# Kernel tuning notes

Measured on AMD Instinct MI355X. Metric: run time of the kernel, lower is better.

## Reference

```python
import jax, jax.numpy as jnp
import numpy as np

KSZ = 3      # kernel_size
NH = 4       # num_heads


def setup_inputs() -> dict:
    key = jax.random.key(0)
    ks = jax.random.split(key, 4)
    B, D, H, W, C = 1, 28, 28, 28, 192
    N = D * H * W
    s = 0.02  # trunc_normal std used by the module's init
    return {
        "x": jax.random.normal(ks[0], (B, N, C), jnp.float32),
        "Wq": jax.random.normal(ks[1], (C, C), jnp.float32) * s,
        "bq": jnp.zeros((C,), jnp.float32),
        "Wkv": jax.random.normal(ks[2], (C, 2 * C), jnp.float32) * s,
        "bkv": jnp.zeros((2 * C,), jnp.float32),
        "Wp": jax.random.normal(ks[3], (C, C), jnp.float32) * s,
        "bp": jnp.zeros((C,), jnp.float32),
        "D": D, "H": H, "W": W,
    }


def _windows(t, D, H, W):
    # t: (B, D+2, H+2, W+2, nh, hc) zero-padded; gather the 27 neighborhood
    # offsets (same flattening order as unfold: d-major, then h, then w).
    return jnp.stack(
        [t[:, dz:dz + D, dy:dy + H, dx:dx + W]
         for dz in range(KSZ) for dy in range(KSZ) for dx in range(KSZ)],
        axis=4)  # (B, D, H, W, 27, nh, hc)


def reference(x, Wq, bq, Wkv, bkv, Wp, bp, D, H, W):
    B, N, C = x.shape
    hc = C // NH
    scale = hc ** (-0.5)
    xv = x.reshape(B, D, H, W, C)

    q = (xv @ Wq + bq).reshape(B, D, H, W, NH, hc) * scale
    kv = (xv @ Wkv + bkv).reshape(B, D, H, W, 2, NH, hc)
    k, v = kv[..., 0, :, :], kv[..., 1, :, :]

    pad = ((0, 0), (1, 1), (1, 1), (1, 1), (0, 0), (0, 0))
    kwin = _windows(jnp.pad(k, pad), D, H, W)  # (B,D,H,W,27,nh,hc)
    vwin = _windows(jnp.pad(v, pad), D, H, W)

    # per-voxel 1x27 attention over the 3x3x3 neighborhood
    attn = jnp.einsum('bdhwnc,bdhwknc->bdhwnk', q, kwin)
    attn = jax.nn.softmax(attn, axis=-1)
    out = jnp.einsum('bdhwnk,bdhwknc->bdhwnc', attn, vwin)
    out = out.reshape(B, D, H, W, C) @ Wp + bp
    return out.reshape(B, N, C)
```

## Files before the change

kernel.cpp:

```cpp
#include <hip/hip_runtime.h>
#include <math.h>

#define CDIM 192
#define DD 28
#define NVOX (DD * DD * DD)

typedef __attribute__((ext_vector_type(8))) short bf16x8;
typedef __attribute__((ext_vector_type(4))) float f32x4;

__device__ __forceinline__ float bf2f(unsigned short u) {
  union { unsigned int i; float f; } w; w.i = ((unsigned int)u) << 16; return w.f;
}
__device__ __forceinline__ float blo(unsigned int u) {
  union { unsigned int i; float f; } w; w.i = u << 16; return w.f;
}
__device__ __forceinline__ float bhi(unsigned int u) {
  union { unsigned int i; float f; } w; w.i = u & 0xffff0000u; return w.f;
}
__device__ __forceinline__ unsigned short f2bf(float f) {
  union { float ff; unsigned int i; } w; w.ff = f;
  unsigned int x = w.i;
  return (unsigned short)((x + 0x7fffu + ((x >> 16) & 1u)) >> 16);
}

__global__ __launch_bounds__(256) void prep(
    const float* __restrict__ x, const float* __restrict__ Wq,
    const float* __restrict__ Wkv, const float* __restrict__ Wp,
    unsigned short* __restrict__ xb, unsigned short* __restrict__ WqT,
    unsigned short* __restrict__ WkvT, unsigned short* __restrict__ WpT)
{
  const int XU = NVOX * CDIM / 8;
  const int t = blockIdx.x * 256 + threadIdx.x;
  if (t < XU) {
    const float4 a = ((const float4*)x)[t * 2];
    const float4 b = ((const float4*)x)[t * 2 + 1];
    unsigned short o[8] = {f2bf(a.x), f2bf(a.y), f2bf(a.z), f2bf(a.w),
                           f2bf(b.x), f2bf(b.y), f2bf(b.z), f2bf(b.w)};
    *(uint4*)(&xb[t * 8]) = *(const uint4*)o;
  } else {
    int u = t - XU;
    if (u < CDIM * CDIM) {
      const int n = u / CDIM, k = u % CDIM;
      WqT[u] = f2bf(Wq[k * CDIM + n]);
    } else if ((u -= CDIM * CDIM) < 2 * CDIM * CDIM) {
      const int n = u / CDIM, k = u % CDIM;
      WkvT[u] = f2bf(Wkv[k * 2 * CDIM + n]);
    } else {
      u -= 2 * CDIM * CDIM;
      const int n = u / CDIM, k = u % CDIM;
      WpT[u] = f2bf(Wp[k * CDIM + n]);
    }
  }
}

template<int OUT_BF16>
__global__ __launch_bounds__(256) void gemm_bf16(
    const unsigned short* __restrict__ A,
    const unsigned short* __restrict__ Bt,
    const float* __restrict__ bias,
    void* __restrict__ Cout,
    int N, float alpha)
{
  __shared__ unsigned short As[64 * 200];
  __shared__ unsigned short Bs[64 * 200];
  const int tid = threadIdx.x;
  const int n0 = blockIdx.x * 64;
  const int m0 = blockIdx.y * 64;

#pragma unroll
  for (int u = tid; u < 1536; u += 256) {
    const int row = u / 24, c = (u % 24) * 8;
    *(uint4*)(&As[row * 200 + c]) =
        *(const uint4*)(&A[(size_t)(m0 + row) * CDIM + c]);
    *(uint4*)(&Bs[row * 200 + c]) =
        *(const uint4*)(&Bt[(size_t)(n0 + row) * CDIM + c]);
  }
  __syncthreads();

  const int l = tid & 63, w = tid >> 6;
  const int wm = (w >> 1) * 32, wn = (w & 1) * 32;
  const int lr = l & 15, lk = (l >> 4) * 8;

  f32x4 acc[2][2] = {};
  const unsigned short* pa = &As[(wm + lr) * 200 + lk];
  const unsigned short* pb = &Bs[(wn + lr) * 200 + lk];

#pragma unroll
  for (int k0 = 0; k0 < CDIM; k0 += 32) {
    const bf16x8 a0 = *(const bf16x8*)(pa + k0);
    const bf16x8 a1 = *(const bf16x8*)(pa + 16 * 200 + k0);
    const bf16x8 b0 = *(const bf16x8*)(pb + k0);
    const bf16x8 b1 = *(const bf16x8*)(pb + 16 * 200 + k0);
    acc[0][0] = __builtin_amdgcn_mfma_f32_16x16x32_bf16(a0, b0, acc[0][0], 0, 0, 0);
    acc[0][1] = __builtin_amdgcn_mfma_f32_16x16x32_bf16(a0, b1, acc[0][1], 0, 0, 0);
    acc[1][0] = __builtin_amdgcn_mfma_f32_16x16x32_bf16(a1, b0, acc[1][0], 0, 0, 0);
    acc[1][1] = __builtin_amdgcn_mfma_f32_16x16x32_bf16(a1, b1, acc[1][1], 0, 0, 0);
  }

#pragma unroll
  for (int i = 0; i < 2; ++i)
#pragma unroll
    for (int j = 0; j < 2; ++j) {
      const int gc = n0 + wn + j * 16 + lr;
      const float bv = bias[gc];
#pragma unroll
      for (int r = 0; r < 4; ++r) {
        const int gr = m0 + wm + i * 16 + (l >> 4) * 4 + r;
        const float v = (acc[i][j][r] + bv) * alpha;
        if (OUT_BF16)
          ((unsigned short*)Cout)[(size_t)gr * N + gc] = f2bf(v);
        else
          ((float*)Cout)[(size_t)gr * N + gc] = v;
      }
    }
}

__global__ __launch_bounds__(256, 4) void attn3d_line(
    const unsigned short* __restrict__ q,
    const unsigned short* __restrict__ kv,
    unsigned short* __restrict__ y)
{
  const int bid = blockIdx.x;
  const int zy = (bid & 7) * 98 + (bid >> 3);
  const int z = zy / 28, yr = zy % 28;
  const int h = threadIdx.x >> 6;
  const int lane = threadIdx.x & 63;
  const int x = lane & 31;
  const int g = lane >> 5;
  const int xc = x < 28 ? x : 27;
  const int cb = h * 48 + g * 24;
  const int vox = (z * 28 + yr) * 28 + xc;

  float qf[24];
  {
    const uint4* qp = (const uint4*)(q + (size_t)vox * CDIM + cb);
    const uint4 a = qp[0], b = qp[1], c = qp[2];
    const unsigned int uu[12] = {a.x, a.y, a.z, a.w, b.x, b.y, b.z, b.w,
                                 c.x, c.y, c.z, c.w};
#pragma unroll
    for (int i = 0; i < 12; ++i) { qf[2*i] = blo(uu[i]); qf[2*i+1] = bhi(uu[i]); }
  }

  const int nx = 3 - (x == 0) - (x == 27);
  const int nyv = 3 - (yr == 0) - (yr == 27);
  const int nzv = 3 - (z == 0) - (z == 27);
  const int noob = 27 - nx * nyv * nzv;
  float m = noob ? 0.f : -INFINITY;
  float s = (float)noob;
  float out[24];
#pragma unroll
  for (int i = 0; i < 24; ++i) out[i] = 0.f;

  const int lm1 = lane - 1, lp1 = lane + 1;
  const bool okm = (x > 0), okp = (x < 27);

  for (int dz = -1; dz <= 1; ++dz) {
    const int zz = z + dz;
    if ((unsigned)zz >= 28u) continue;
    for (int dy = -1; dy <= 1; ++dy) {
      const int yv = yr + dy;
      if ((unsigned)yv >= 28u) continue;
      const unsigned short* row =
          kv + (size_t)((zz * 28 + yv) * 28 + xc) * (2 * CDIM) + cb;
      const uint4* kp = (const uint4*)row;
      const uint4* vp = (const uint4*)(row + CDIM);
      const uint4 ka = kp[0], kb = kp[1], kc = kp[2];
      const uint4 va = vp[0], vb = vp[1], vc = vp[2];
      const unsigned int ku[12] = {ka.x, ka.y, ka.z, ka.w, kb.x, kb.y, kb.z,
                                   kb.w, kc.x, kc.y, kc.z, kc.w};
      const unsigned int vu[12] = {va.x, va.y, va.z, va.w, vb.x, vb.y, vb.z,
                                   vb.w, vc.x, vc.y, vc.z, vc.w};

      float p0 = 0.f, p1 = 0.f, p2 = 0.f;
#pragma unroll
      for (int i = 0; i < 12; ++i) {
        p1 += qf[2*i] * blo(ku[i]) + qf[2*i+1] * bhi(ku[i]);
        unsigned int t = (unsigned int)__shfl((int)ku[i], lm1);
        p0 += qf[2*i] * blo(t) + qf[2*i+1] * bhi(t);
        t = (unsigned int)__shfl((int)ku[i], lp1);
        p2 += qf[2*i] * blo(t) + qf[2*i+1] * bhi(t);
      }
      p0 += __shfl_xor(p0, 32);
      p1 += __shfl_xor(p1, 32);
      p2 += __shfl_xor(p2, 32);

      const float l0 = okm ? p0 : -INFINITY;
      const float l2 = okp ? p2 : -INFINITY;
      const float nm = fmaxf(m, fmaxf(p1, fmaxf(l0, l2)));
      const float sc = __expf(m - nm);
      const float w0 = okm ? __expf(p0 - nm) : 0.f;
      const float w1 = __expf(p1 - nm);
      const float w2 = okp ? __expf(p2 - nm) : 0.f;
      s = s * sc + w0 + w1 + w2;
      m = nm;

#pragma unroll
      for (int i = 0; i < 12; ++i) {
        const unsigned int am = (unsigned int)__shfl((int)vu[i], lm1);
        const unsigned int ap = (unsigned int)__shfl((int)vu[i], lp1);
        out[2*i]   = out[2*i]   * sc + w0 * blo(am) + w1 * blo(vu[i]) + w2 * blo(ap);
        out[2*i+1] = out[2*i+1] * sc + w0 * bhi(am) + w1 * bhi(vu[i]) + w2 * bhi(ap);
      }
    }
  }

  if (x < 28) {
    const float inv = 1.f / s;
    unsigned int ou[12];
#pragma unroll
    for (int i = 0; i < 12; ++i)
      ou[i] = (unsigned int)f2bf(out[2*i] * inv) |
              ((unsigned int)f2bf(out[2*i+1] * inv) << 16);
    uint4* yp = (uint4*)(y + (size_t)vox * CDIM + cb);
    yp[0] = make_uint4(ou[0], ou[1], ou[2], ou[3]);
    yp[1] = make_uint4(ou[4], ou[5], ou[6], ou[7]);
    yp[2] = make_uint4(ou[8], ou[9], ou[10], ou[11]);
  }
}

extern "C" void kernel_launch(void* const* d_in, const int* in_sizes, int n_in,
                              void* d_out, int out_size, void* d_ws, size_t ws_size,
                              hipStream_t stream) {
  const float* x   = (const float*)d_in[0];
  const float* Wq  = (const float*)d_in[1];
  const float* bq  = (const float*)d_in[2];
  const float* Wkv = (const float*)d_in[3];
  const float* bkv = (const float*)d_in[4];
  const float* Wp  = (const float*)d_in[5];
  const float* bp  = (const float*)d_in[6];
  float* out = (float*)d_out;

  unsigned short* xb   = (unsigned short*)d_ws;
  unsigned short* WqT  = xb + (size_t)NVOX * CDIM;
  unsigned short* WkvT = WqT + CDIM * CDIM;
  unsigned short* WpT  = WkvT + 2 * CDIM * CDIM;
  unsigned short* qb   = WpT + CDIM * CDIM;
  unsigned short* kvb  = qb + (size_t)NVOX * CDIM;
  unsigned short* yb   = kvb + (size_t)NVOX * 2 * CDIM;

  const float scale = 1.0f / sqrtf(48.0f);

  prep<<<674304 / 256, 256, 0, stream>>>(x, Wq, Wkv, Wp, xb, WqT, WkvT, WpT);

  gemm_bf16<1><<<dim3(CDIM / 64, NVOX / 64), 256, 0, stream>>>(
      xb, WqT, bq, qb, CDIM, scale);
  gemm_bf16<1><<<dim3(2 * CDIM / 64, NVOX / 64), 256, 0, stream>>>(
      xb, WkvT, bkv, kvb, 2 * CDIM, 1.0f);
  attn3d_line<<<DD * DD, 256, 0, stream>>>(qb, kvb, yb);
  gemm_bf16<0><<<dim3(CDIM / 64, NVOX / 64), 256, 0, stream>>>(
      yb, WpT, bp, out, CDIM, 1.0f);
}
```

Baseline: 147.5 us.

## Fuse x conversion into merged QKV GEMM and software-pipeline attention row loads

Removes the separate pass that converts x to bf16 and instead converts fp32 x into shared memory inside a merged QKV GEMM. That GEMM reuses each A tile across several N tiles, with the attention scale folded into the prepared weights and biases. The attention kernel now double-buffers K/V row loads across the nine neighbor rows, loading the next row before computing the current one, and drops the occupancy hint from launch bounds. This cuts global traffic and launches, but the QKV GEMM has fewer blocks with serialized N tiles, and the attention kernel uses more registers.

```diff
diff --git a/kernel.cpp b/kernel.cpp
--- a/kernel.cpp
+++ b/kernel.cpp
@@ -8,9 +8,6 @@
 typedef __attribute__((ext_vector_type(8))) short bf16x8;
 typedef __attribute__((ext_vector_type(4))) float f32x4;
 
-__device__ __forceinline__ float bf2f(unsigned short u) {
-  union { unsigned int i; float f; } w; w.i = ((unsigned int)u) << 16; return w.f;
-}
 __device__ __forceinline__ float blo(unsigned int u) {
   union { unsigned int i; float f; } w; w.i = u << 16; return w.f;
 }
@@ -23,99 +20,151 @@
   return (unsigned short)((x + 0x7fffu + ((x >> 16) & 1u)) >> 16);
 }
 
-__global__ __launch_bounds__(256) void prep(
-    const float* __restrict__ x, const float* __restrict__ Wq,
-    const float* __restrict__ Wkv, const float* __restrict__ Wp,
-    unsigned short* __restrict__ xb, unsigned short* __restrict__ WqT,
-    unsigned short* __restrict__ WkvT, unsigned short* __restrict__ WpT)
+__global__ __launch_bounds__(256) void prep_w(
+    const float* __restrict__ Wq, const float* __restrict__ Wkv,
+    const float* __restrict__ Wp, const float* __restrict__ bq,
+    const float* __restrict__ bkv,
+    unsigned short* __restrict__ WqkvT, unsigned short* __restrict__ WpT,
+    float* __restrict__ biasAll, float scale)
 {
-  const int XU = NVOX * CDIM / 8;
-  const int t = blockIdx.x * 256 + threadIdx.x;
-  if (t < XU) {
-    const float4 a = ((const float4*)x)[t * 2];
-    const float4 b = ((const float4*)x)[t * 2 + 1];
-    unsigned short o[8] = {f2bf(a.x), f2bf(a.y), f2bf(a.z), f2bf(a.w),
-                           f2bf(b.x), f2bf(b.y), f2bf(b.z), f2bf(b.w)};
-    *(uint4*)(&xb[t * 8]) = *(const uint4*)o;
-  } else {
-    int u = t - XU;
-    if (u < CDIM * CDIM) {
-      const int n = u / CDIM, k = u % CDIM;
-      WqT[u] = f2bf(Wq[k * CDIM + n]);
-    } else if ((u -= CDIM * CDIM) < 2 * CDIM * CDIM) {
-      const int n = u / CDIM, k = u % CDIM;
-      WkvT[u] = f2bf(Wkv[k * 2 * CDIM + n]);
-    } else {
-      u -= 2 * CDIM * CDIM;
-      const int n = u / CDIM, k = u % CDIM;
-      WpT[u] = f2bf(Wp[k * CDIM + n]);
-    }
-  }
-}
-
-template<int OUT_BF16>
-__global__ __launch_bounds__(256) void gemm_bf16(
-    const unsigned short* __restrict__ A,
+  int t = blockIdx.x * 256 + threadIdx.x;
+  if (t < 576 * CDIM) {
+    const int n = t / CDIM, k = t % CDIM;
+    const float v = (n < CDIM) ? Wq[k * CDIM + n] * scale
+                               : Wkv[k * 2 * CDIM + (n - CDIM)];
+    WqkvT[t] = f2bf(v);
+    return;
+  }
+  t -= 576 * CDIM;
+  if (t < CDIM * CDIM) {
+    const int n = t / CDIM, k = t % CDIM;
+    WpT[t] = f2bf(Wp[k * CDIM + n]);
+    return;
+  }
+  t -= CDIM * CDIM;
+  if (t < 576)
+    biasAll[t] = (t < CDIM) ? bq[t] * scale : bkv[t - CDIM];
+}
+
+__global__ __launch_bounds__(256) void gemm_qkv(
+    const float* __restrict__ X,
     const unsigned short* __restrict__ Bt,
-    const float* __restrict__ bias,
-    void* __restrict__ Cout,
-    int N, float alpha)
+    const float* __restrict__ biasAll,
+    unsigned short* __restrict__ qb,
+    unsigned short* __restrict__ kvb)
 {
   __shared__ unsigned short As[64 * 200];
   __shared__ unsigned short Bs[64 * 200];
   const int tid = threadIdx.x;
-  const int n0 = blockIdx.x * 64;
-  const int m0 = blockIdx.y * 64;
+  const int m0 = blockIdx.x * 64;
+  const int by = blockIdx.y;
 
 #pragma unroll
   for (int u = tid; u < 1536; u += 256) {
     const int row = u / 24, c = (u % 24) * 8;
-    *(uint4*)(&As[row * 200 + c]) =
-        *(const uint4*)(&A[(size_t)(m0 + row) * CDIM + c]);
-    *(uint4*)(&Bs[row * 200 + c]) =
-        *(const uint4*)(&Bt[(size_t)(n0 + row) * CDIM + c]);
-  }
-  __syncthreads();
+    const float4 f0 = *(const float4*)(&X[(size_t)(m0 + row) * CDIM + c]);
+    const float4 f1 = *(const float4*)(&X[(size_t)(m0 + row) * CDIM + c + 4]);
+    unsigned short o[8] = {f2bf(f0.x), f2bf(f0.y), f2bf(f0.z), f2bf(f0.w),
+                           f2bf(f1.x), f2bf(f1.y), f2bf(f1.z), f2bf(f1.w)};
+    *(uint4*)(&As[row * 200 + c]) = *(const uint4*)o;
+  }
 
   const int l = tid & 63, w = tid >> 6;
   const int wm = (w >> 1) * 32, wn = (w & 1) * 32;
   const int lr = l & 15, lk = (l >> 4) * 8;
-
-  f32x4 acc[2][2] = {};
   const unsigned short* pa = &As[(wm + lr) * 200 + lk];
   const unsigned short* pb = &Bs[(wn + lr) * 200 + lk];
 
-#pragma unroll
-  for (int k0 = 0; k0 < CDIM; k0 += 32) {
-    const bf16x8 a0 = *(const bf16x8*)(pa + k0);
-    const bf16x8 a1 = *(const bf16x8*)(pa + 16 * 200 + k0);
-    const bf16x8 b0 = *(const bf16x8*)(pb + k0);
-    const bf16x8 b1 = *(const bf16x8*)(pb + 16 * 200 + k0);
-    acc[0][0] = __builtin_amdgcn_mfma_f32_16x16x32_bf16(a0, b0, acc[0][0], 0, 0, 0);
-    acc[0][1] = __builtin_amdgcn_mfma_f32_16x16x32_bf16(a0, b1, acc[0][1], 0, 0, 0);
-    acc[1][0] = __builtin_amdgcn_mfma_f32_16x16x32_bf16(a1, b0, acc[1][0], 0, 0, 0);
-    acc[1][1] = __builtin_amdgcn_mfma_f32_16x16x32_bf16(a1, b1, acc[1][1], 0, 0, 0);
-  }
-
-#pragma unroll
-  for (int i = 0; i < 2; ++i)
-#pragma unroll
-    for (int j = 0; j < 2; ++j) {
-      const int gc = n0 + wn + j * 16 + lr;
-      const float bv = bias[gc];
-#pragma unroll
-      for (int r = 0; r < 4; ++r) {
-        const int gr = m0 + wm + i * 16 + (l >> 4) * 4 + r;
-        const float v = (acc[i][j][r] + bv) * alpha;
-        if (OUT_BF16)
-          ((unsigned short*)Cout)[(size_t)gr * N + gc] = f2bf(v);
-        else
-          ((float*)Cout)[(size_t)gr * N + gc] = v;
+  for (int nt = by; nt < 9; nt += 2) {
+    const int n0 = nt * 64;
+    __syncthreads();
+#pragma unroll
+    for (int u = tid; u < 1536; u += 256) {
+      const int row = u / 24, c = (u % 24) * 8;
+      *(uint4*)(&Bs[row * 200 + c]) =
+          *(const uint4*)(&Bt[(size_t)(n0 + row) * CDIM + c]);
+    }
+    __syncthreads();
+
+    f32x4 acc[2][2] = {};
+#pragma unroll
+    for (int k0 = 0; k0 < CDIM; k0 += 32) {
+      const bf16x8 a0 = *(const bf16x8*)(pa + k0);
+      const bf16x8 a1 = *(const bf16x8*)(pa + 16 * 200 + k0);
+      const bf16x8 b0 = *(const bf16x8*)(pb + k0);
+      const bf16x8 b1 = *(const bf16x8*)(pb + 16 * 200 + k0);
+      acc[0][0] = __builtin_amdgcn_mfma_f32_16x16x32_bf16(a0, b0, acc[0][0], 0, 0, 0);
+      acc[0][1] = __builtin_amdgcn_mfma_f32_16x16x32_bf16(a0, b1, acc[0][1], 0, 0, 0);
+      acc[1][0] = __builtin_amdgcn_mfma_f32_16x16x32_bf16(a1, b0, acc[1][0], 0, 0, 0);
+      acc[1][1] = __builtin_amdgcn_mfma_f32_16x16x32_bf16(a1, b1, acc[1][1], 0, 0, 0);
+    }
+
+#pragma unroll
+    for (int i = 0; i < 2; ++i)
+#pragma unroll
+      for (int j = 0; j < 2; ++j) {
+        const int gc = n0 + wn + j * 16 + lr;
+        const float bv = biasAll[gc];
+#pragma unroll
+        for (int r = 0; r < 4; ++r) {
+          const int gr = m0 + wm + i * 16 + (l >> 4) * 4 + r;
+          const float v = acc[i][j][r] + bv;
+          if (gc < CDIM)
+            qb[(size_t)gr * CDIM + gc] = f2bf(v);
+          else
+            kvb[(size_t)gr * 2 * CDIM + (gc - CDIM)] = f2bf(v);
+        }
       }
-    }
-}
-
-__global__ __launch_bounds__(256, 4) void attn3d_line(
+  }
+}
+
+__device__ __forceinline__ void load_row(const unsigned short* rp,
+    uint4& K0, uint4& K1, uint4& K2, uint4& V0, uint4& V1, uint4& V2) {
+  const uint4* kp = (const uint4*)rp;
+  const uint4* vp = (const uint4*)(rp + CDIM);
+  K0 = kp[0]; K1 = kp[1]; K2 = kp[2];
+  V0 = vp[0]; V1 = vp[1]; V2 = vp[2];
+}
+
+__device__ __forceinline__ void do_row(
+    uint4 K0, uint4 K1, uint4 K2, uint4 V0, uint4 V1, uint4 V2,
+    const float* __restrict__ qf, float* __restrict__ out,
+    float& m, float& s, int lm1, int lp1, bool okm, bool okp) {
+  const unsigned int ku[12] = {K0.x, K0.y, K0.z, K0.w, K1.x, K1.y, K1.z, K1.w,
+                               K2.x, K2.y, K2.z, K2.w};
+  const unsigned int vu[12] = {V0.x, V0.y, V0.z, V0.w, V1.x, V1.y, V1.z, V1.w,
+                               V2.x, V2.y, V2.z, V2.w};
+  float p0 = 0.f, p1 = 0.f, p2 = 0.f;
+#pragma unroll
+  for (int i = 0; i < 12; ++i) {
+    p1 += qf[2*i] * blo(ku[i]) + qf[2*i+1] * bhi(ku[i]);
+    unsigned int t = (unsigned int)__shfl((int)ku[i], lm1);
+    p0 += qf[2*i] * blo(t) + qf[2*i+1] * bhi(t);
+    t = (unsigned int)__shfl((int)ku[i], lp1);
+    p2 += qf[2*i] * blo(t) + qf[2*i+1] * bhi(t);
+  }
+  p0 += __shfl_xor(p0, 32);
+  p1 += __shfl_xor(p1, 32);
+  p2 += __shfl_xor(p2, 32);
+  const float l0 = okm ? p0 : -INFINITY;
+  const float l2 = okp ? p2 : -INFINITY;
+  const float nm = fmaxf(m, fmaxf(p1, fmaxf(l0, l2)));
+  const float sc = __expf(m - nm);
+  const float w0 = okm ? __expf(p0 - nm) : 0.f;
+  const float w1 = __expf(p1 - nm);
+  const float w2 = okp ? __expf(p2 - nm) : 0.f;
+  s = s * sc + w0 + w1 + w2;
+  m = nm;
+#pragma unroll
+  for (int i = 0; i < 12; ++i) {
+    const unsigned int am = (unsigned int)__shfl((int)vu[i], lm1);
+    const unsigned int ap = (unsigned int)__shfl((int)vu[i], lp1);
+    out[2*i]   = out[2*i]   * sc + w0 * blo(am) + w1 * blo(vu[i]) + w2 * blo(ap);
+    out[2*i+1] = out[2*i+1] * sc + w0 * bhi(am) + w1 * bhi(vu[i]) + w2 * bhi(ap);
+  }
+}
+
+__global__ __launch_bounds__(256) void attn3d_line(
     const unsigned short* __restrict__ q,
     const unsigned short* __restrict__ kv,
     unsigned short* __restrict__ y)
@@ -154,55 +203,38 @@
   const int lm1 = lane - 1, lp1 = lane + 1;
   const bool okm = (x > 0), okp = (x < 27);
 
-  for (int dz = -1; dz <= 1; ++dz) {
-    const int zz = z + dz;
-    if ((unsigned)zz >= 28u) continue;
-    for (int dy = -1; dy <= 1; ++dy) {
-      const int yv = yr + dy;
-      if ((unsigned)yv >= 28u) continue;
-      const unsigned short* row =
-          kv + (size_t)((zz * 28 + yv) * 28 + xc) * (2 * CDIM) + cb;
-      const uint4* kp = (const uint4*)row;
-      const uint4* vp = (const uint4*)(row + CDIM);
-      const uint4 ka = kp[0], kb = kp[1], kc = kp[2];
-      const uint4 va = vp[0], vb = vp[1], vc = vp[2];
-      const unsigned int ku[12] = {ka.x, ka.y, ka.z, ka.w, kb.x, kb.y, kb.z,
-                                   kb.w, kc.x, kc.y, kc.z, kc.w};
-      const unsigned int vu[12] = {va.x, va.y, va.z, va.w, vb.x, vb.y, vb.z,
-                                   vb.w, vc.x, vc.y, vc.z, vc.w};
-
-      float p0 = 0.f, p1 = 0.f, p2 = 0.f;
-#pragma unroll
-      for (int i = 0; i < 12; ++i) {
-        p1 += qf[2*i] * blo(ku[i]) + qf[2*i+1] * bhi(ku[i]);
-        unsigned int t = (unsigned int)__shfl((int)ku[i], lm1);
-        p0 += qf[2*i] * blo(t) + qf[2*i+1] * bhi(t);
-        t = (unsigned int)__shfl((int)ku[i], lp1);
-        p2 += qf[2*i] * blo(t) + qf[2*i+1] * bhi(t);
-      }
-      p0 += __shfl_xor(p0, 32);
-      p1 += __shfl_xor(p1, 32);
-      p2 += __shfl_xor(p2, 32);
-
-      const float l0 = okm ? p0 : -INFINITY;
-      const float l2 = okp ? p2 : -INFINITY;
-      const float nm = fmaxf(m, fmaxf(p1, fmaxf(l0, l2)));
-      const float sc = __expf(m - nm);
-      const float w0 = okm ? __expf(p0 - nm) : 0.f;
-      const float w1 = __expf(p1 - nm);
-      const float w2 = okp ? __expf(p2 - nm) : 0.f;
-      s = s * sc + w0 + w1 + w2;
-      m = nm;
-
-#pragma unroll
-      for (int i = 0; i < 12; ++i) {
-        const unsigned int am = (unsigned int)__shfl((int)vu[i], lm1);
-        const unsigned int ap = (unsigned int)__shfl((int)vu[i], lp1);
-        out[2*i]   = out[2*i]   * sc + w0 * blo(am) + w1 * blo(vu[i]) + w2 * blo(ap);
-        out[2*i+1] = out[2*i+1] * sc + w0 * bhi(am) + w1 * bhi(vu[i]) + w2 * bhi(ap);
-      }
-    }
-  }
+  const unsigned short* rbase = kv + (size_t)xc * 384 + cb;
+  const int zm = z > 0 ? z - 1 : 0,  zp = z < 27 ? z + 1 : 27;
+  const int ym = yr > 0 ? yr - 1 : 0, yp = yr < 27 ? yr + 1 : 27;
+  const int r0 = (zm*28+ym)*10752, r1 = (zm*28+yr)*10752, r2 = (zm*28+yp)*10752;
+  const int r3 = (z *28+ym)*10752, r4 = (z *28+yr)*10752, r5 = (z *28+yp)*10752;
+  const int r6 = (zp*28+ym)*10752, r7 = (zp*28+yr)*10752, r8 = (zp*28+yp)*10752;
+  const bool vz0 = z > 0, vz2 = z < 27, vy0 = yr > 0, vy2 = yr < 27;
+  const bool v0 = vz0 && vy0, v1 = vz0, v2 = vz0 && vy2;
+  const bool v3 = vy0,                  v5 = vy2;
+  const bool v6 = vz2 && vy0, v7 = vz2, v8 = vz2 && vy2;
+
+  uint4 Ak0, Ak1, Ak2, Av0, Av1, Av2;
+  uint4 Bk0, Bk1, Bk2, Bv0, Bv1, Bv2;
+
+  load_row(rbase + r0, Ak0, Ak1, Ak2, Av0, Av1, Av2);
+  load_row(rbase + r1, Bk0, Bk1, Bk2, Bv0, Bv1, Bv2);
+  if (v0) do_row(Ak0, Ak1, Ak2, Av0, Av1, Av2, qf, out, m, s, lm1, lp1, okm, okp);
+  load_row(rbase + r2, Ak0, Ak1, Ak2, Av0, Av1, Av2);
+  if (v1) do_row(Bk0, Bk1, Bk2, Bv0, Bv1, Bv2, qf, out, m, s, lm1, lp1, okm, okp);
+  load_row(rbase + r3, Bk0, Bk1, Bk2, Bv0, Bv1, Bv2);
+  if (v2) do_row(Ak0, Ak1, Ak2, Av0, Av1, Av2, qf, out, m, s, lm1, lp1, okm, okp);
+  load_row(rbase + r4, Ak0, Ak1, Ak2, Av0, Av1, Av2);
+  if (v3) do_row(Bk0, Bk1, Bk2, Bv0, Bv1, Bv2, qf, out, m, s, lm1, lp1, okm, okp);
+  load_row(rbase + r5, Bk0, Bk1, Bk2, Bv0, Bv1, Bv2);
+  do_row(Ak0, Ak1, Ak2, Av0, Av1, Av2, qf, out, m, s, lm1, lp1, okm, okp);
+  load_row(rbase + r6, Ak0, Ak1, Ak2, Av0, Av1, Av2);
+  if (v5) do_row(Bk0, Bk1, Bk2, Bv0, Bv1, Bv2, qf, out, m, s, lm1, lp1, okm, okp);
+  load_row(rbase + r7, Bk0, Bk1, Bk2, Bv0, Bv1, Bv2);
+  if (v6) do_row(Ak0, Ak1, Ak2, Av0, Av1, Av2, qf, out, m, s, lm1, lp1, okm, okp);
+  load_row(rbase + r8, Ak0, Ak1, Ak2, Av0, Av1, Av2);
+  if (v7) do_row(Bk0, Bk1, Bk2, Bv0, Bv1, Bv2, qf, out, m, s, lm1, lp1, okm, okp);
+  if (v8) do_row(Ak0, Ak1, Ak2, Av0, Av1, Av2, qf, out, m, s, lm1, lp1, okm, okp);
 
   if (x < 28) {
     const float inv = 1.f / s;
@@ -216,6 +248,62 @@
     yp[1] = make_uint4(ou[4], ou[5], ou[6], ou[7]);
     yp[2] = make_uint4(ou[8], ou[9], ou[10], ou[11]);
   }
+}
+
+__global__ __launch_bounds__(256) void gemm_out(
+    const unsigned short* __restrict__ A,
+    const unsigned short* __restrict__ Bt,
+    const float* __restrict__ bias,
+    float* __restrict__ C)
+{
+  __shared__ unsigned short As[64 * 200];
+  __shared__ unsigned short Bs[64 * 200];
+  const int tid = threadIdx.x;
+  const int n0 = blockIdx.x * 64;
+  const int m0 = blockIdx.y * 64;
+
+#pragma unroll
+  for (int u = tid; u < 1536; u += 256) {
+    const int row = u / 24, c = (u % 24) * 8;
+    *(uint4*)(&As[row * 200 + c]) =
+        *(const uint4*)(&A[(size_t)(m0 + row) * CDIM + c]);
+    *(uint4*)(&Bs[row * 200 + c]) =
+        *(const uint4*)(&Bt[(size_t)(n0 + row) * CDIM + c]);
+  }
+  __syncthreads();
+
+  const int l = tid & 63, w = tid >> 6;
+  const int wm = (w >> 1) * 32, wn = (w & 1) * 32;
+  const int lr = l & 15, lk = (l >> 4) * 8;
+
+  f32x4 acc[2][2] = {};
+  const unsigned short* pa = &As[(wm + lr) * 200 + lk];
+  const unsigned short* pb = &Bs[(wn + lr) * 200 + lk];
+
+#pragma unroll
+  for (int k0 = 0; k0 < CDIM; k0 += 32) {
+    const bf16x8 a0 = *(const bf16x8*)(pa + k0);
+    const bf16x8 a1 = *(const bf16x8*)(pa + 16 * 200 + k0);
+    const bf16x8 b0 = *(const bf16x8*)(pb + k0);
+    const bf16x8 b1 = *(const bf16x8*)(pb + 16 * 200 + k0);
+    acc[0][0] = __builtin_amdgcn_mfma_f32_16x16x32_bf16(a0, b0, acc[0][0], 0, 0, 0);
+    acc[0][1] = __builtin_amdgcn_mfma_f32_16x16x32_bf16(a0, b1, acc[0][1], 0, 0, 0);
+    acc[1][0] = __builtin_amdgcn_mfma_f32_16x16x32_bf16(a1, b0, acc[1][0], 0, 0, 0);
+    acc[1][1] = __builtin_amdgcn_mfma_f32_16x16x32_bf16(a1, b1, acc[1][1], 0, 0, 0);
+  }
+
+#pragma unroll
+  for (int i = 0; i < 2; ++i)
+#pragma unroll
+    for (int j = 0; j < 2; ++j) {
+      const int gc = n0 + wn + j * 16 + lr;
+      const float bv = bias[gc];
+#pragma unroll
+      for (int r = 0; r < 4; ++r) {
+        const int gr = m0 + wm + i * 16 + (l >> 4) * 4 + r;
+        C[(size_t)gr * CDIM + gc] = acc[i][j][r] + bv;
+      }
+    }
 }
 
 extern "C" void kernel_launch(void* const* d_in, const int* in_sizes, int n_in,
@@ -230,23 +318,19 @@
   const float* bp  = (const float*)d_in[6];
   float* out = (float*)d_out;
 
-  unsigned short* xb   = (unsigned short*)d_ws;
-  unsigned short* WqT  = xb + (size_t)NVOX * CDIM;
-  unsigned short* WkvT = WqT + CDIM * CDIM;
-  unsigned short* WpT  = WkvT + 2 * CDIM * CDIM;
-  unsigned short* qb   = WpT + CDIM * CDIM;
-  unsigned short* kvb  = qb + (size_t)NVOX * CDIM;
-  unsigned short* yb   = kvb + (size_t)NVOX * 2 * CDIM;
+  unsigned short* WqkvT = (unsigned short*)d_ws;
+  unsigned short* WpT   = WqkvT + 576 * CDIM;
+  float*          biasA = (float*)(WpT + CDIM * CDIM);
+  unsigned short* qb    = (unsigned short*)(biasA + 576);
+  unsigned short* kvb   = qb + (size_t)NVOX * CDIM;
+  unsigned short* yb    = kvb + (size_t)NVOX * 2 * CDIM;
 
   const float scale = 1.0f / sqrtf(48.0f);
 
-  prep<<<674304 / 256, 256, 0, stream>>>(x, Wq, Wkv, Wp, xb, WqT, WkvT, WpT);
-
-  gemm_bf16<1><<<dim3(CDIM / 64, NVOX / 64), 256, 0, stream>>>(
-      xb, WqT, bq, qb, CDIM, scale);
-  gemm_bf16<1><<<dim3(2 * CDIM / 64, NVOX / 64), 256, 0, stream>>>(
-      xb, WkvT, bkv, kvb, 2 * CDIM, 1.0f);
+  prep_w<<<(148032 + 255) / 256, 256, 0, stream>>>(
+      Wq, Wkv, Wp, bq, bkv, WqkvT, WpT, biasA, scale);
+
+  gemm_qkv<<<dim3(NVOX / 64, 2), 256, 0, stream>>>(x, WqkvT, biasA, qb, kvb);
   attn3d_line<<<DD * DD, 256, 0, stream>>>(qb, kvb, yb);
-  gemm_bf16<0><<<dim3(CDIM / 64, NVOX / 64), 256, 0, stream>>>(
-      yb, WpT, bp, out, CDIM, 1.0f);
-}
+  gemm_out<<<dim3(3, NVOX / 64), 256, 0, stream>>>(yb, WpT, bp, out);
+}
```

Result: no change. 146.9 us (-0.4%).
